# Optimization experiments

Hardware: AMD Instinct MI355X
Metric: run time of the kernel (lower is better)

## Reference

```python
import jax, jax.numpy as jnp
import numpy as np

B, S, D, H = 2, 4096, 512, 8
HD = D // H  # 64


def setup_inputs() -> dict:
    key = jax.random.key(0)
    ks = jax.random.split(key, 9)
    def lin_init(kw, kb, fan_in, fan_out):
        bound = 1.0 / np.sqrt(fan_in)
        W = jax.random.uniform(kw, (fan_in, fan_out), minval=-bound, maxval=bound, dtype=jnp.float32)
        b = jax.random.uniform(kb, (fan_out,), minval=-bound, maxval=bound, dtype=jnp.float32)
        return W, b
    Wq, bq = lin_init(ks[0], ks[1], D, D)
    Wk, bk = lin_init(ks[2], ks[3], D, D)
    Wv, bv = lin_init(ks[4], ks[5], D, D)
    query = jax.random.normal(ks[6], (B, S, D), dtype=jnp.float32)
    key_in = jax.random.normal(ks[7], (B, S, D), dtype=jnp.float32)
    value = jax.random.normal(ks[8], (B, S, D), dtype=jnp.float32)
    return {"query": query, "key": key_in, "value": value,
            "Wq": Wq, "bq": bq, "Wk": Wk, "bk": bk, "Wv": Wv, "bv": bv}


def _split_heads(x):
    # [B, S, D] -> [B, H, S, HD]
    b, s, _ = x.shape
    return x.reshape(b, s, H, HD).transpose(0, 2, 1, 3)


def reference(query, key, value, Wq, bq, Wk, bk, Wv, bv):
    Q = _split_heads(query @ Wq + bq)
    K = _split_heads(key @ Wk + bk)
    V = _split_heads(value @ Wv + bv)
    scale = 1.0 / np.sqrt(HD).astype(np.float32)
    # scores: [B, H, Sq, Sk]
    scores = jnp.einsum('bhqd,bhkd->bhqk', Q, K) * scale
    weights = jax.nn.softmax(scores, axis=-1)
    att = jnp.einsum('bhqk,bhkd->bhqd', weights, V)
    # [B, H, S, HD] -> [B, S, D]
    return att.transpose(0, 2, 1, 3).reshape(query.shape[0], query.shape[1], D)
```

## Files before the change

kernel.cpp:

```cpp
#include <hip/hip_runtime.h>
#include <hip/hip_bf16.h>
#include <cstdint>


typedef __bf16   bf16x8 __attribute__((ext_vector_type(8)));
typedef _Float16 f16x8  __attribute__((ext_vector_type(8)));
typedef float    f32x4  __attribute__((ext_vector_type(4)));
typedef float    f32x16 __attribute__((ext_vector_type(16)));
typedef unsigned int   u32;
typedef unsigned int   u32x4 __attribute__((ext_vector_type(4)));
typedef unsigned short u16;

#define NB  2
#define SEQ 4096
#define DIM 512
#define NH  8
#define HD  64
#define WSZ (DIM * DIM)
#define XSZ (NB * SEQ * DIM)
#define QSZ (NB * NH * SEQ * HD)

__device__ __forceinline__ u16 f2bf(float f) {
    __bf16 h = (__bf16)f; return __builtin_bit_cast(u16, h);
}
__device__ __forceinline__ u16 f2h(float f) {
    _Float16 h = (_Float16)f; return __builtin_bit_cast(u16, h);
}
__device__ __forceinline__ u32 pack_pkrtz(float a, float b) {
    auto pk = __builtin_amdgcn_cvt_pkrtz(a, b);
    return __builtin_bit_cast(u32, pk);
}
__device__ __forceinline__ bf16x8 cvt8p(float4 a, float4 b) {
    bf16x8 o;
    o[0]=(__bf16)a.x; o[1]=(__bf16)a.y; o[2]=(__bf16)a.z; o[3]=(__bf16)a.w;
    o[4]=(__bf16)b.x; o[5]=(__bf16)b.y; o[6]=(__bf16)b.z; o[7]=(__bf16)b.w;
    return o;
}
__device__ __forceinline__ void dma16(const u16* g, u16* l) {
    __builtin_amdgcn_global_load_lds(
        (const __attribute__((address_space(1))) u32*)g,
        (__attribute__((address_space(3))) u32*)l, 16, 0, 0);
}

__global__ __launch_bounds__(256) void xcvt_kernel(
    const float* __restrict__ xq, const float* __restrict__ xk,
    const float* __restrict__ xv, u16* __restrict__ xb)
{
    const int id = blockIdx.x;
    const int p = id >> 10, rest = id & 1023;
    const int mtile = rest >> 4, kk = rest & 15;
    const float* X = (p == 0) ? xq : ((p == 1) ? xk : xv);
    const int t = threadIdx.x;
    const int row = t >> 1, half = t & 1;
    const float* src = X + ((size_t)(mtile * 128 + row)) * DIM + kk * 32 + half * 16;
    u16* dst = xb + (size_t)p * XSZ + ((size_t)(mtile * 16 + kk)) * 4096 + row * 32;
    const int sr = (row ^ (row >> 2)) & 3;
    float4 a0 = ((const float4*)src)[0], a1 = ((const float4*)src)[1];
    float4 a2 = ((const float4*)src)[2], a3 = ((const float4*)src)[3];
    const int c0 = (half * 2) ^ sr, c1 = (half * 2 + 1) ^ sr;
    *(bf16x8*)(dst + (c0 << 3)) = cvt8p(a0, a1);
    *(bf16x8*)(dst + (c1 << 3)) = cvt8p(a2, a3);
}

__global__ __launch_bounds__(256) void wt_kernel(
    const float* __restrict__ Wq, const float* __restrict__ Wk,
    const float* __restrict__ Wv, u16* __restrict__ wtImg)
{
    __shared__ u16 lT[64 * 65];
    const int p = blockIdx.z;
    const float* W = (p == 0) ? Wq : ((p == 1) ? Wk : Wv);
    const int r0 = blockIdx.x * 64, c0 = blockIdx.y * 64;
    const int t = threadIdx.x;
#pragma unroll
    for (int i = 0; i < 16; i++) {
        int idx = i * 256 + t, rowk = idx >> 6, coln = idx & 63;
        lT[coln * 65 + rowk] = f2bf(W[(size_t)(r0 + rowk) * DIM + c0 + coln]);
    }
    __syncthreads();
#pragma unroll
    for (int i = 0; i < 2; i++) {
        const int idx = i * 256 + t;
        const int nl = idx >> 3, ch = idx & 7;
        const int n = c0 + nl;
        const int row = n & 127, ntile = n >> 7;
        const int kk = (r0 >> 5) + (ch >> 2);
        const int sw = (ch & 3) ^ ((row ^ (row >> 2)) & 3);
        u16* d = wtImg + (size_t)p * WSZ + ((size_t)(ntile * 16 + kk)) * 4096
               + row * 32 + (sw << 3);
#pragma unroll
        for (int e = 0; e < 8; e++) d[e] = lT[nl * 65 + ch * 8 + e];
    }
}

__global__ __launch_bounds__(256) void proj_kernel(
    const u16* __restrict__ xb, const u16* __restrict__ wtImg,
    const float* __restrict__ bq, const float* __restrict__ bk,
    const float* __restrict__ bv,
    u16* __restrict__ qb, u16* __restrict__ kbImg, u16* __restrict__ vtImg)
{
    __shared__ u16 smem[16384];

    const int tid = threadIdx.x;
    const int wave = tid >> 6, lane = tid & 63;
    const int l16 = lane & 15, quad = lane >> 4;
    const int wq = wave >> 1, wn = wave & 1;

    const int id = blockIdx.x;
    const int xcd = id & 7, j = id >> 3;
    const int p = j >> 5, t5 = j & 31;
    int mb, nb;
    if (p < 2) { mb = xcd * 8 + (t5 >> 2); nb = t5 & 3; }
    else       { nb = xcd * 8 + (t5 >> 2); mb = t5 & 3; }

    const u16* Abase = (p < 2) ? xb + (size_t)p * XSZ + (size_t)mb * 16 * 4096
                               : wtImg + (size_t)2 * WSZ + (size_t)mb * 16 * 4096;
    const u16* Bbase = (p < 2) ? wtImg + (size_t)p * WSZ + (size_t)nb * 16 * 4096
                               : xb + (size_t)2 * XSZ + (size_t)nb * 16 * 4096;
    const int doff = tid * 8;

    f32x4 acc[4][4];
#pragma unroll
    for (int ms = 0; ms < 4; ms++)
#pragma unroll
        for (int ns = 0; ns < 4; ns++)
#pragma unroll
            for (int jj = 0; jj < 4; jj++) acc[ms][ns][jj] = 0.f;

#pragma unroll
    for (int e = 0; e < 2; e++) {
        dma16(Abase + e * 2048 + doff, smem + e * 2048 + doff);
        dma16(Bbase + e * 2048 + doff, smem + 4096 + e * 2048 + doff);
    }
    Abase += 4096; Bbase += 4096;

    for (int kt = 0; kt < 16; kt++) {
        __syncthreads();
        if (kt < 15) {
            u16* lb = smem + ((kt + 1) & 1) * 8192;
#pragma unroll
            for (int e = 0; e < 2; e++) {
                dma16(Abase + e * 2048 + doff, lb + e * 2048 + doff);
                dma16(Bbase + e * 2048 + doff, lb + 4096 + e * 2048 + doff);
            }
            Abase += 4096; Bbase += 4096;
        }
        const u16* lA = smem + (kt & 1) * 8192;
        const u16* lB = lA + 4096;

        bf16x8 af[4];
#pragma unroll
        for (int ms = 0; ms < 4; ms++) {
            const int row = wq * 64 + ms * 16 + l16;
            const int sr = (row ^ (row >> 2)) & 3;
            af[ms] = *(const bf16x8*)&lA[row * 32 + ((quad ^ sr) << 3)];
        }
#pragma unroll
        for (int ns = 0; ns < 4; ns++) {
            const int rowb = wn * 64 + ns * 16 + l16;
            const int sb = (rowb ^ (rowb >> 2)) & 3;
            const bf16x8 b = *(const bf16x8*)&lB[rowb * 32 + ((quad ^ sb) << 3)];
#pragma unroll
            for (int ms = 0; ms < 4; ms++)
                acc[ms][ns] = __builtin_amdgcn_mfma_f32_16x16x32_bf16(af[ms], b, acc[ms][ns], 0, 0, 0);
        }
    }

    __syncthreads();
    if (p < 2) {
        const float* bias = p ? bk : bq;
        const float cs = (p == 0) ? 0.18033688011112042f : 1.0f;
        const int stl = wn * 2 + wq;
        const int hh = nb * 2 + wn;
#pragma unroll
        for (int ns = 0; ns < 4; ns++) {
            const int ch = ns * 16 + l16;
            const float bval = bias[hh * 64 + ch];
#pragma unroll
            for (int ms = 0; ms < 4; ms++)
#pragma unroll
                for (int rr = 0; rr < 4; rr++) {
                    const int sqL = ms * 16 + quad * 4 + rr;
                    const float v = (acc[ms][ns][rr] + bval) * cs;
                    int off;
                    if (p == 0) off = sqL * 64 + ch;
                    else        off = sqL * 64 +
                                      (((ch >> 3) ^ ((sqL ^ (sqL >> 3)) & 7)) << 3) + (ch & 7);
                    smem[stl * 4096 + off] = f2bf(v);
                }
        }
    } else {
        const int stl = wq * 2 + wn;
#pragma unroll
        for (int ms = 0; ms < 4; ms++)
#pragma unroll
            for (int rr = 0; rr < 4; rr++) {
                const int hd = ms * 16 + quad * 4 + rr;
                const float bval = bv[mb * 128 + wq * 64 + hd];
                const int swh = (hd ^ (hd >> 3)) & 7;
#pragma unroll
                for (int ns = 0; ns < 4; ns++) {
                    const int nl = ns * 16 + l16;
                    const int sqpL = (nl & ~12) | ((nl & 8) >> 1) | ((nl & 4) << 1);
                    smem[stl * 4096 + hd * 64 +
                         (((sqpL >> 3) ^ swh) << 3) + (sqpL & 7)] =
                        f2h(acc[ms][ns][rr] + bval);
                }
            }
    }
    __syncthreads();

    {
        u16* dstp; size_t gbase;
        if (p < 2) {
            const int hh = nb * 2 + (wave >> 1);
            const int b2 = mb >> 5;
            const int row0 = (mb * 128 + (wave & 1) * 64) & 4095;
            if (p == 0) { dstp = qb;    gbase = ((size_t)(b2 * NH + hh) * 4096 + row0) * 64; }
            else        { dstp = kbImg; gbase = ((size_t)((b2 * NH + hh) * 64 + (row0 >> 6))) * 4096; }
        } else {
            const int hh = mb * 2 + (wave >> 1);
            const int b2 = nb >> 5;
            const int nblk = (nb & 31) * 2 + (wave & 1);
            dstp = vtImg; gbase = ((size_t)((b2 * NH + hh) * 64 + nblk)) * 4096;
        }
#pragma unroll
        for (int e = 0; e < 8; e++) {
            const u32x4 vv = *(const u32x4*)&smem[wave * 4096 + e * 512 + lane * 8];
            *(u32x4*)(dstp + gbase + e * 512 + lane * 8) = vv;
        }
    }
}

__global__ __launch_bounds__(512, 4) void attn_kernel(
    const u16* __restrict__ qb, const u16* __restrict__ kbImg,
    const u16* __restrict__ vtImg, float* __restrict__ out)
{
    __shared__ u16 smem[2 * 4 * 4096];
    float* cmb = (float*)smem;

    const int tid = threadIdx.x;
    const int wave = tid >> 6, lane = tid & 63;
    const int m31 = lane & 31, h = lane >> 5;
    const int wq = wave >> 1, kh = wave & 1;

    const int blk = blockIdx.x;
    const int xcd = blk & 7, idx = blk >> 3;
    const int bh = xcd * 2 + (idx >> 5);
    const int qt = idx & 31;
    const int qbase = qt * 128 + wq * 32;

    bf16x8 qF[4];
#pragma unroll
    for (int c = 0; c < 4; c++)
        qF[c] = *(const bf16x8*)(qb + ((size_t)bh * SEQ + qbase + m31) * HD + c * 16 + h * 8);

    f32x16 O0, O1;
#pragma unroll
    for (int j = 0; j < 16; j++) { O0[j] = 0.f; O1[j] = 0.f; }
    float l_acc = 0.f;

    const int st  = wave >> 1;
    const int hw  = wave & 1;
    const u16* img = (st & 1) ? vtImg : kbImg;
    const u16* gp = img + ((size_t)(bh * 64 + (st >> 1) * 32)) * 4096 + hw * 2048 + lane * 8;
    {
        u16* lb = smem + st * 4096 + hw * 2048 + lane * 8;
#pragma unroll
        for (int e = 0; e < 4; e++) dma16(gp + e * 512, lb + e * 512);
        gp += 4096;
    }

    const int NT = 32;
    for (int it = 0; it < NT; it++) {
        __syncthreads();
        if (it + 1 < NT) {
            u16* lb = smem + ((((it + 1) & 1) * 4 + st)) * 4096 + hw * 2048 + lane * 8;
#pragma unroll
            for (int e = 0; e < 4; e++) dma16(gp + e * 512, lb + e * 512);
            gp += 4096;
        }
        const u16* sK = smem + (size_t)(((it & 1) * 4) + kh * 2) * 4096;
        const u16* sV = sK + 4096;

#pragma unroll
        for (int kg = 0; kg < 2; kg++) {
            const int rK = kg * 32 + m31;
            const int swK = (rK ^ (rK >> 3)) & 7;
            bf16x8 kA[4];
#pragma unroll
            for (int c = 0; c < 4; c++)
                kA[c] = *(const bf16x8*)&sK[(rK << 6) + (((2 * c + h) ^ swK) << 3)];

            const int swV0 = (m31 ^ (m31 >> 3)) & 7;
            const int rV1 = 32 + m31;
            const int swV1 = (rV1 ^ (rV1 >> 3)) & 7;
            f16x8 vA0[2], vA1[2];
#pragma unroll
            for (int c2 = 0; c2 < 2; c2++) {
                vA0[c2] = *(const f16x8*)&sV[(m31 << 6) + (((4 * kg + 2 * c2 + h) ^ swV0) << 3)];
                vA1[c2] = *(const f16x8*)&sV[(rV1 << 6) + (((4 * kg + 2 * c2 + h) ^ swV1) << 3)];
            }

            f32x16 Sv;
#pragma unroll
            for (int j = 0; j < 16; j++) Sv[j] = 0.f;
#pragma unroll
            for (int c = 0; c < 4; c++)
                Sv = __builtin_amdgcn_mfma_f32_32x32x16_bf16(kA[c], qF[c], Sv, 0, 0, 0);

            float ps = 0.f;
            u32 P32[8];
#pragma unroll
            for (int mm = 0; mm < 8; mm++) {
                const float e0 = __builtin_amdgcn_exp2f(Sv[2 * mm]);
                const float e1 = __builtin_amdgcn_exp2f(Sv[2 * mm + 1]);
                ps += e0 + e1;
                P32[mm] = pack_pkrtz(e0, e1);
            }
            l_acc += ps;

            u32x4 f0, f1;
            f0[0] = P32[0]; f0[1] = P32[1]; f0[2] = P32[2]; f0[3] = P32[3];
            f1[0] = P32[4]; f1[1] = P32[5]; f1[2] = P32[6]; f1[3] = P32[7];
            const f16x8 pf0 = __builtin_bit_cast(f16x8, f0);
            const f16x8 pf1 = __builtin_bit_cast(f16x8, f1);
            O0 = __builtin_amdgcn_mfma_f32_32x32x16_f16(vA0[0], pf0, O0, 0, 0, 0);
            O0 = __builtin_amdgcn_mfma_f32_32x32x16_f16(vA0[1], pf1, O0, 0, 0, 0);
            O1 = __builtin_amdgcn_mfma_f32_32x32x16_f16(vA1[0], pf0, O1, 0, 0, 0);
            O1 = __builtin_amdgcn_mfma_f32_32x32x16_f16(vA1[1], pf1, O1, 0, 0, 0);
        }
    }

    l_acc += __shfl_xor(l_acc, 32);
    __syncthreads();
    if (kh == 1) {
#pragma unroll
        for (int hg = 0; hg < 2; hg++)
#pragma unroll
            for (int mm = 0; mm < 4; mm++) {
                f32x4 o;
#pragma unroll
                for (int j = 0; j < 4; j++) o[j] = (hg ? O1 : O0)[4 * mm + j];
                *(f32x4*)&cmb[(((wq * 2 + hg) * 4 + mm) << 8) + lane * 4] = o;
            }
        cmb[8192 + wq * 64 + lane] = l_acc;
    }
    __syncthreads();

    if (kh == 0) {
        const int b = bh >> 3, hcol = bh & 7;
        const float lt = l_acc + cmb[8192 + wq * 64 + lane];
        const float inv = 1.0f / lt;
        const int sq = qbase + m31;
#pragma unroll
        for (int hg = 0; hg < 2; hg++)
#pragma unroll
            for (int mm = 0; mm < 4; mm++) {
                const f32x4 po = *(const f32x4*)&cmb[(((wq * 2 + hg) * 4 + mm) << 8) + lane * 4];
                f32x4 o;
#pragma unroll
                for (int j = 0; j < 4; j++)
                    o[j] = ((hg ? O1 : O0)[4 * mm + j] + po[j]) * inv;
                *(f32x4*)&out[(((size_t)(b * SEQ + sq)) << 9) + hcol * 64
                              + hg * 32 + 8 * mm + 4 * h] = o;
            }
    }
}

extern "C" void kernel_launch(void* const* d_in, const int* in_sizes, int n_in,
                              void* d_out, int out_size, void* d_ws, size_t ws_size,
                              hipStream_t stream)
{
    const float* q  = (const float*)d_in[0];
    const float* k  = (const float*)d_in[1];
    const float* v  = (const float*)d_in[2];
    const float* Wq = (const float*)d_in[3];
    const float* bq = (const float*)d_in[4];
    const float* Wk = (const float*)d_in[5];
    const float* bk = (const float*)d_in[6];
    const float* Wv = (const float*)d_in[7];
    const float* bv = (const float*)d_in[8];
    float* out = (float*)d_out;

    u16* xb  = (u16*)d_ws;
    u16* wti = xb  + (size_t)3 * XSZ;
    u16* qbp = wti + (size_t)3 * WSZ;
    u16* kbp = qbp + (size_t)QSZ;
    u16* vtp = kbp + (size_t)QSZ;

    xcvt_kernel<<<dim3(3072),   256, 0, stream>>>(q, k, v, xb);
    wt_kernel  <<<dim3(8, 8, 3), 256, 0, stream>>>(Wq, Wk, Wv, wti);
    proj_kernel<<<dim3(768),    256, 0, stream>>>(xb, wti, bq, bk, bv,
                                                  qbp, kbp, vtp);
    attn_kernel<<<dim3(512),    512, 0, stream>>>(qbp, kbp, vtp, out);
}
```

Before: 211.2 us.

## Split attention KV work across 4 waves per query tile and merge prep kernels

Attention blocks grow from 512 to 1024 threads, so each query group is served by four key-split waves instead of two. Each wave handles one 32-key sub-tile per iteration rather than looping over two, which gives more waves to hide latency. The partial outputs and row sums are combined with a two-stage reduction through shared memory. The input-conversion and weight-transpose kernels are merged into one launch, MFMA sections get s_setprio hints, and the row sum is accumulated with fdot2 on the packed f16 probabilities. In exchange, the reduction epilogue is larger and the launch bounds put more register pressure on each thread.

```diff
diff --git a/kernel.cpp b/kernel.cpp
--- a/kernel.cpp
+++ b/kernel.cpp
@@ -5,6 +5,7 @@
 
 typedef __bf16   bf16x8 __attribute__((ext_vector_type(8)));
 typedef _Float16 f16x8  __attribute__((ext_vector_type(8)));
+typedef _Float16 f16x2  __attribute__((ext_vector_type(2)));
 typedef float    f32x4  __attribute__((ext_vector_type(4)));
 typedef float    f32x16 __attribute__((ext_vector_type(16)));
 typedef unsigned int   u32;
@@ -20,6 +21,12 @@
 #define XSZ (NB * SEQ * DIM)
 #define QSZ (NB * NH * SEQ * HD)
 
+#if __has_builtin(__builtin_amdgcn_fdot2)
+#define HAVE_FDOT2 1
+#else
+#define HAVE_FDOT2 0
+#endif
+
 __device__ __forceinline__ u16 f2bf(float f) {
     __bf16 h = (__bf16)f; return __builtin_bit_cast(u16, h);
 }
@@ -42,53 +49,53 @@
         (__attribute__((address_space(3))) u32*)l, 16, 0, 0);
 }
 
-__global__ __launch_bounds__(256) void xcvt_kernel(
+__global__ __launch_bounds__(256) void prep_kernel(
     const float* __restrict__ xq, const float* __restrict__ xk,
-    const float* __restrict__ xv, u16* __restrict__ xb)
-{
-    const int id = blockIdx.x;
-    const int p = id >> 10, rest = id & 1023;
-    const int mtile = rest >> 4, kk = rest & 15;
-    const float* X = (p == 0) ? xq : ((p == 1) ? xk : xv);
-    const int t = threadIdx.x;
-    const int row = t >> 1, half = t & 1;
-    const float* src = X + ((size_t)(mtile * 128 + row)) * DIM + kk * 32 + half * 16;
-    u16* dst = xb + (size_t)p * XSZ + ((size_t)(mtile * 16 + kk)) * 4096 + row * 32;
-    const int sr = (row ^ (row >> 2)) & 3;
-    float4 a0 = ((const float4*)src)[0], a1 = ((const float4*)src)[1];
-    float4 a2 = ((const float4*)src)[2], a3 = ((const float4*)src)[3];
-    const int c0 = (half * 2) ^ sr, c1 = (half * 2 + 1) ^ sr;
-    *(bf16x8*)(dst + (c0 << 3)) = cvt8p(a0, a1);
-    *(bf16x8*)(dst + (c1 << 3)) = cvt8p(a2, a3);
-}
-
-__global__ __launch_bounds__(256) void wt_kernel(
+    const float* __restrict__ xv,
     const float* __restrict__ Wq, const float* __restrict__ Wk,
-    const float* __restrict__ Wv, u16* __restrict__ wtImg)
+    const float* __restrict__ Wv,
+    u16* __restrict__ xb, u16* __restrict__ wtImg)
 {
     __shared__ u16 lT[64 * 65];
-    const int p = blockIdx.z;
-    const float* W = (p == 0) ? Wq : ((p == 1) ? Wk : Wv);
-    const int r0 = blockIdx.x * 64, c0 = blockIdx.y * 64;
+    const int id = blockIdx.x;
     const int t = threadIdx.x;
-#pragma unroll
-    for (int i = 0; i < 16; i++) {
-        int idx = i * 256 + t, rowk = idx >> 6, coln = idx & 63;
-        lT[coln * 65 + rowk] = f2bf(W[(size_t)(r0 + rowk) * DIM + c0 + coln]);
-    }
-    __syncthreads();
-#pragma unroll
-    for (int i = 0; i < 2; i++) {
-        const int idx = i * 256 + t;
-        const int nl = idx >> 3, ch = idx & 7;
-        const int n = c0 + nl;
-        const int row = n & 127, ntile = n >> 7;
-        const int kk = (r0 >> 5) + (ch >> 2);
-        const int sw = (ch & 3) ^ ((row ^ (row >> 2)) & 3);
-        u16* d = wtImg + (size_t)p * WSZ + ((size_t)(ntile * 16 + kk)) * 4096
-               + row * 32 + (sw << 3);
-#pragma unroll
-        for (int e = 0; e < 8; e++) d[e] = lT[nl * 65 + ch * 8 + e];
+    if (id < 3072) {
+        const int p = id >> 10, rest = id & 1023;
+        const int mtile = rest >> 4, kk = rest & 15;
+        const float* X = (p == 0) ? xq : ((p == 1) ? xk : xv);
+        const int row = t >> 1, half = t & 1;
+        const float* src = X + ((size_t)(mtile * 128 + row)) * DIM + kk * 32 + half * 16;
+        u16* dst = xb + (size_t)p * XSZ + ((size_t)(mtile * 16 + kk)) * 4096 + row * 32;
+        const int sr = (row ^ (row >> 2)) & 3;
+        float4 a0 = ((const float4*)src)[0], a1 = ((const float4*)src)[1];
+        float4 a2 = ((const float4*)src)[2], a3 = ((const float4*)src)[3];
+        const int c0 = (half * 2) ^ sr, c1 = (half * 2 + 1) ^ sr;
+        *(bf16x8*)(dst + (c0 << 3)) = cvt8p(a0, a1);
+        *(bf16x8*)(dst + (c1 << 3)) = cvt8p(a2, a3);
+    } else {
+        const int id2 = id - 3072;
+        const int p = id2 >> 6;
+        const float* W = (p == 0) ? Wq : ((p == 1) ? Wk : Wv);
+        const int r0 = ((id2 >> 3) & 7) * 64, c0 = (id2 & 7) * 64;
+#pragma unroll
+        for (int i = 0; i < 16; i++) {
+            int idx = i * 256 + t, rowk = idx >> 6, coln = idx & 63;
+            lT[coln * 65 + rowk] = f2bf(W[(size_t)(r0 + rowk) * DIM + c0 + coln]);
+        }
+        __syncthreads();
+#pragma unroll
+        for (int i = 0; i < 2; i++) {
+            const int idx = i * 256 + t;
+            const int nl = idx >> 3, ch = idx & 7;
+            const int n = c0 + nl;
+            const int row = n & 127, ntile = n >> 7;
+            const int kk = (r0 >> 5) + (ch >> 2);
+            const int sw = (ch & 3) ^ ((row ^ (row >> 2)) & 3);
+            u16* d = wtImg + (size_t)p * WSZ + ((size_t)(ntile * 16 + kk)) * 4096
+                   + row * 32 + (sw << 3);
+#pragma unroll
+            for (int e = 0; e < 8; e++) d[e] = lT[nl * 65 + ch * 8 + e];
+        }
     }
 }
 
@@ -231,17 +238,17 @@
     }
 }
 
-__global__ __launch_bounds__(512, 4) void attn_kernel(
+__global__ __launch_bounds__(1024, 8) void attn_kernel(
     const u16* __restrict__ qb, const u16* __restrict__ kbImg,
     const u16* __restrict__ vtImg, float* __restrict__ out)
 {
-    __shared__ u16 smem[2 * 4 * 4096];
-    float* cmb = (float*)smem;
+    __shared__ u16 smem[2 * 16384];
+    float* sf = (float*)smem;
 
     const int tid = threadIdx.x;
     const int wave = tid >> 6, lane = tid & 63;
     const int m31 = lane & 31, h = lane >> 5;
-    const int wq = wave >> 1, kh = wave & 1;
+    const int wq = wave >> 2, kh = wave & 3;
 
     const int blk = blockIdx.x;
     const int xcd = blk & 7, idx = blk >> 3;
@@ -257,106 +264,139 @@
     f32x16 O0, O1;
 #pragma unroll
     for (int j = 0; j < 16; j++) { O0[j] = 0.f; O1[j] = 0.f; }
-    float l_acc = 0.f;
-
-    const int st  = wave >> 1;
-    const int hw  = wave & 1;
-    const u16* img = (st & 1) ? vtImg : kbImg;
-    const u16* gp = img + ((size_t)(bh * 64 + (st >> 1) * 32)) * 4096 + hw * 2048 + lane * 8;
-    {
-        u16* lb = smem + st * 4096 + hw * 2048 + lane * 8;
-#pragma unroll
-        for (int e = 0; e < 4; e++) dma16(gp + e * 512, lb + e * 512);
-        gp += 4096;
-    }
+    float la_ = 0.f, lb_ = 0.f;
+#if HAVE_FDOT2
+    const f16x2 one2 = {(_Float16)1.f, (_Float16)1.f};
+#endif
+
+    const int region = wave >> 3, sub8 = wave & 7;
+    const u16* img = region ? vtImg : kbImg;
+    const u16* gp = img + ((size_t)(bh * 64)) * 4096 + sub8 * 1024 + lane * 8;
+    u16* const lds0 = smem + region * 8192 + sub8 * 1024 + lane * 8;
+
+    dma16(gp, lds0); dma16(gp + 512, lds0 + 512);
+    gp += 8192;
 
     const int NT = 32;
     for (int it = 0; it < NT; it++) {
         __syncthreads();
         if (it + 1 < NT) {
-            u16* lb = smem + ((((it + 1) & 1) * 4 + st)) * 4096 + hw * 2048 + lane * 8;
-#pragma unroll
-            for (int e = 0; e < 4; e++) dma16(gp + e * 512, lb + e * 512);
-            gp += 4096;
-        }
-        const u16* sK = smem + (size_t)(((it & 1) * 4) + kh * 2) * 4096;
-        const u16* sV = sK + 4096;
-
-#pragma unroll
-        for (int kg = 0; kg < 2; kg++) {
-            const int rK = kg * 32 + m31;
-            const int swK = (rK ^ (rK >> 3)) & 7;
-            bf16x8 kA[4];
-#pragma unroll
-            for (int c = 0; c < 4; c++)
-                kA[c] = *(const bf16x8*)&sK[(rK << 6) + (((2 * c + h) ^ swK) << 3)];
-
-            const int swV0 = (m31 ^ (m31 >> 3)) & 7;
-            const int rV1 = 32 + m31;
-            const int swV1 = (rV1 ^ (rV1 >> 3)) & 7;
-            f16x8 vA0[2], vA1[2];
-#pragma unroll
-            for (int c2 = 0; c2 < 2; c2++) {
-                vA0[c2] = *(const f16x8*)&sV[(m31 << 6) + (((4 * kg + 2 * c2 + h) ^ swV0) << 3)];
-                vA1[c2] = *(const f16x8*)&sV[(rV1 << 6) + (((4 * kg + 2 * c2 + h) ^ swV1) << 3)];
+            u16* ld = lds0 + ((it + 1) & 1) * 16384;
+            dma16(gp, ld); dma16(gp + 512, ld + 512);
+            gp += 8192;
+        }
+        const u16* sb = smem + (it & 1) * 16384;
+        const u16* sK = sb + ((kh >> 1) << 12);
+        const u16* sV = sb + 8192 + ((kh >> 1) << 12);
+
+        const int rK = ((kh & 1) << 5) + m31;
+        const int swK = (rK ^ (rK >> 3)) & 7;
+        bf16x8 kA[4];
+#pragma unroll
+        for (int c = 0; c < 4; c++)
+            kA[c] = *(const bf16x8*)&sK[(rK << 6) + (((2 * c + h) ^ swK) << 3)];
+
+        f32x16 Sv;
+#pragma unroll
+        for (int j = 0; j < 16; j++) Sv[j] = 0.f;
+        __builtin_amdgcn_s_setprio(1);
+#pragma unroll
+        for (int c = 0; c < 4; c++)
+            Sv = __builtin_amdgcn_mfma_f32_32x32x16_bf16(kA[c], qF[c], Sv, 0, 0, 0);
+        __builtin_amdgcn_s_setprio(0);
+
+        const int gb = (kh & 1) << 2;
+        const int swV0 = (m31 ^ (m31 >> 3)) & 7;
+        const int rV1 = 32 + m31;
+        const int swV1 = (rV1 ^ (rV1 >> 3)) & 7;
+        f16x8 vA0[2], vA1[2];
+#pragma unroll
+        for (int c2 = 0; c2 < 2; c2++) {
+            vA0[c2] = *(const f16x8*)&sV[(m31 << 6) + (((gb + 2 * c2 + h) ^ swV0) << 3)];
+            vA1[c2] = *(const f16x8*)&sV[(rV1 << 6) + (((gb + 2 * c2 + h) ^ swV1) << 3)];
+        }
+
+        u32 P32[8];
+#pragma unroll
+        for (int mm = 0; mm < 8; mm++) {
+            const float ea = __builtin_amdgcn_exp2f(Sv[2 * mm]);
+            const float eb = __builtin_amdgcn_exp2f(Sv[2 * mm + 1]);
+            P32[mm] = pack_pkrtz(ea, eb);
+#if HAVE_FDOT2
+            const f16x2 pp = __builtin_bit_cast(f16x2, P32[mm]);
+            if (mm & 1) lb_ = __builtin_amdgcn_fdot2(pp, one2, lb_, false);
+            else        la_ = __builtin_amdgcn_fdot2(pp, one2, la_, false);
+#else
+            if (mm & 1) lb_ += ea + eb; else la_ += ea + eb;
+#endif
+        }
+
+        u32x4 f0, f1;
+        f0[0] = P32[0]; f0[1] = P32[1]; f0[2] = P32[2]; f0[3] = P32[3];
+        f1[0] = P32[4]; f1[1] = P32[5]; f1[2] = P32[6]; f1[3] = P32[7];
+        const f16x8 pf0 = __builtin_bit_cast(f16x8, f0);
+        const f16x8 pf1 = __builtin_bit_cast(f16x8, f1);
+        __builtin_amdgcn_s_setprio(1);
+        O0 = __builtin_amdgcn_mfma_f32_32x32x16_f16(vA0[0], pf0, O0, 0, 0, 0);
+        O0 = __builtin_amdgcn_mfma_f32_32x32x16_f16(vA0[1], pf1, O0, 0, 0, 0);
+        O1 = __builtin_amdgcn_mfma_f32_32x32x16_f16(vA1[0], pf0, O1, 0, 0, 0);
+        O1 = __builtin_amdgcn_mfma_f32_32x32x16_f16(vA1[1], pf1, O1, 0, 0, 0);
+        __builtin_amdgcn_s_setprio(0);
+    }
+
+    float l_acc = la_ + lb_;
+    l_acc += __shfl_xor(l_acc, 32);
+
+    if (lane < 32) sf[wave * 32 + lane] = l_acc;
+    __syncthreads();
+    const float lt = sf[(wq * 4 + 0) * 32 + m31] + sf[(wq * 4 + 1) * 32 + m31]
+                   + sf[(wq * 4 + 2) * 32 + m31] + sf[(wq * 4 + 3) * 32 + m31];
+    const float inv = 1.0f / lt;
+    __syncthreads();
+
+    if (kh >= 2) {
+        const int w2 = wq * 2 + (kh - 2);
+#pragma unroll
+        for (int s = 0; s < 8; s++) {
+            f32x4 tv;
+#pragma unroll
+            for (int j = 0; j < 4; j++) tv[j] = (s < 4 ? O0 : O1)[(s & 3) * 4 + j];
+            *(f32x4*)&sf[w2 * 2048 + s * 256 + lane * 4] = tv;
+        }
+    }
+    __syncthreads();
+    if (kh < 2) {
+        const int w2 = wq * 2 + kh;
+#pragma unroll
+        for (int s = 0; s < 8; s++) {
+            const f32x4 tv = *(const f32x4*)&sf[w2 * 2048 + s * 256 + lane * 4];
+#pragma unroll
+            for (int j = 0; j < 4; j++) {
+                if (s < 4) O0[(s & 3) * 4 + j] += tv[j];
+                else       O1[(s & 3) * 4 + j] += tv[j];
             }
-
-            f32x16 Sv;
-#pragma unroll
-            for (int j = 0; j < 16; j++) Sv[j] = 0.f;
-#pragma unroll
-            for (int c = 0; c < 4; c++)
-                Sv = __builtin_amdgcn_mfma_f32_32x32x16_bf16(kA[c], qF[c], Sv, 0, 0, 0);
-
-            float ps = 0.f;
-            u32 P32[8];
-#pragma unroll
-            for (int mm = 0; mm < 8; mm++) {
-                const float e0 = __builtin_amdgcn_exp2f(Sv[2 * mm]);
-                const float e1 = __builtin_amdgcn_exp2f(Sv[2 * mm + 1]);
-                ps += e0 + e1;
-                P32[mm] = pack_pkrtz(e0, e1);
-            }
-            l_acc += ps;
-
-            u32x4 f0, f1;
-            f0[0] = P32[0]; f0[1] = P32[1]; f0[2] = P32[2]; f0[3] = P32[3];
-            f1[0] = P32[4]; f1[1] = P32[5]; f1[2] = P32[6]; f1[3] = P32[7];
-            const f16x8 pf0 = __builtin_bit_cast(f16x8, f0);
-            const f16x8 pf1 = __builtin_bit_cast(f16x8, f1);
-            O0 = __builtin_amdgcn_mfma_f32_32x32x16_f16(vA0[0], pf0, O0, 0, 0, 0);
-            O0 = __builtin_amdgcn_mfma_f32_32x32x16_f16(vA0[1], pf1, O0, 0, 0, 0);
-            O1 = __builtin_amdgcn_mfma_f32_32x32x16_f16(vA1[0], pf0, O1, 0, 0, 0);
-            O1 = __builtin_amdgcn_mfma_f32_32x32x16_f16(vA1[1], pf1, O1, 0, 0, 0);
-        }
-    }
-
-    l_acc += __shfl_xor(l_acc, 32);
+        }
+    }
     __syncthreads();
     if (kh == 1) {
 #pragma unroll
-        for (int hg = 0; hg < 2; hg++)
-#pragma unroll
-            for (int mm = 0; mm < 4; mm++) {
-                f32x4 o;
-#pragma unroll
-                for (int j = 0; j < 4; j++) o[j] = (hg ? O1 : O0)[4 * mm + j];
-                *(f32x4*)&cmb[(((wq * 2 + hg) * 4 + mm) << 8) + lane * 4] = o;
-            }
-        cmb[8192 + wq * 64 + lane] = l_acc;
-    }
-    __syncthreads();
-
+        for (int s = 0; s < 8; s++) {
+            f32x4 tv;
+#pragma unroll
+            for (int j = 0; j < 4; j++) tv[j] = (s < 4 ? O0 : O1)[(s & 3) * 4 + j];
+            *(f32x4*)&sf[wq * 2048 + s * 256 + lane * 4] = tv;
+        }
+    }
+    __syncthreads();
     if (kh == 0) {
         const int b = bh >> 3, hcol = bh & 7;
-        const float lt = l_acc + cmb[8192 + wq * 64 + lane];
-        const float inv = 1.0f / lt;
         const int sq = qbase + m31;
 #pragma unroll
         for (int hg = 0; hg < 2; hg++)
 #pragma unroll
             for (int mm = 0; mm < 4; mm++) {
-                const f32x4 po = *(const f32x4*)&cmb[(((wq * 2 + hg) * 4 + mm) << 8) + lane * 4];
+                const int s = hg * 4 + mm;
+                const f32x4 po = *(const f32x4*)&sf[wq * 2048 + s * 256 + lane * 4];
                 f32x4 o;
 #pragma unroll
                 for (int j = 0; j < 4; j++)
@@ -388,9 +428,8 @@
     u16* kbp = qbp + (size_t)QSZ;
     u16* vtp = kbp + (size_t)QSZ;
 
-    xcvt_kernel<<<dim3(3072),   256, 0, stream>>>(q, k, v, xb);
-    wt_kernel  <<<dim3(8, 8, 3), 256, 0, stream>>>(Wq, Wk, Wv, wti);
-    proj_kernel<<<dim3(768),    256, 0, stream>>>(xb, wti, bq, bk, bv,
-                                                  qbp, kbp, vtp);
-    attn_kernel<<<dim3(512),    512, 0, stream>>>(qbp, kbp, vtp, out);
-}
+    prep_kernel<<<dim3(3264), 256, 0, stream>>>(q, k, v, Wq, Wk, Wv, xb, wti);
+    proj_kernel<<<dim3(768),  256, 0, stream>>>(xb, wti, bq, bk, bv,
+                                                qbp, kbp, vtp);
+    attn_kernel<<<dim3(512), 1024, 0, stream>>>(qbp, kbp, vtp, out);
+}
```

Measured after the change: 771.7 us. 3.65x slower.

## Merge prep kernels and software-pipeline QK/PV MFMAs in attention loop

Applied to the files above, without the earlier changes.

Merges the input-conversion and weight-transpose kernels into one launch, removing a kernel launch and its tail. In the attention inner loop, the two key groups are manually unrolled so the second group's QK MFMAs are interleaved with the first group's PV MFMAs. MFMA sections are wrapped in s_setprio, and the row-sum is accumulated with fdot2 on packed fp16 into two accumulators. The aim is to overlap exp/VALU work with matrix ops and cut launch overhead. The costs are higher register pressure and slightly different rounding in the row-sum.

```diff
diff --git a/kernel.cpp b/kernel.cpp
--- a/kernel.cpp
+++ b/kernel.cpp
@@ -5,6 +5,7 @@
 
 typedef __bf16   bf16x8 __attribute__((ext_vector_type(8)));
 typedef _Float16 f16x8  __attribute__((ext_vector_type(8)));
+typedef _Float16 f16x2  __attribute__((ext_vector_type(2)));
 typedef float    f32x4  __attribute__((ext_vector_type(4)));
 typedef float    f32x16 __attribute__((ext_vector_type(16)));
 typedef unsigned int   u32;
@@ -20,6 +21,12 @@
 #define XSZ (NB * SEQ * DIM)
 #define QSZ (NB * NH * SEQ * HD)
 
+#if __has_builtin(__builtin_amdgcn_fdot2)
+#define HAVE_FDOT2 1
+#else
+#define HAVE_FDOT2 0
+#endif
+
 __device__ __forceinline__ u16 f2bf(float f) {
     __bf16 h = (__bf16)f; return __builtin_bit_cast(u16, h);
 }
@@ -42,53 +49,53 @@
         (__attribute__((address_space(3))) u32*)l, 16, 0, 0);
 }
 
-__global__ __launch_bounds__(256) void xcvt_kernel(
+__global__ __launch_bounds__(256) void prep_kernel(
     const float* __restrict__ xq, const float* __restrict__ xk,
-    const float* __restrict__ xv, u16* __restrict__ xb)
-{
-    const int id = blockIdx.x;
-    const int p = id >> 10, rest = id & 1023;
-    const int mtile = rest >> 4, kk = rest & 15;
-    const float* X = (p == 0) ? xq : ((p == 1) ? xk : xv);
-    const int t = threadIdx.x;
-    const int row = t >> 1, half = t & 1;
-    const float* src = X + ((size_t)(mtile * 128 + row)) * DIM + kk * 32 + half * 16;
-    u16* dst = xb + (size_t)p * XSZ + ((size_t)(mtile * 16 + kk)) * 4096 + row * 32;
-    const int sr = (row ^ (row >> 2)) & 3;
-    float4 a0 = ((const float4*)src)[0], a1 = ((const float4*)src)[1];
-    float4 a2 = ((const float4*)src)[2], a3 = ((const float4*)src)[3];
-    const int c0 = (half * 2) ^ sr, c1 = (half * 2 + 1) ^ sr;
-    *(bf16x8*)(dst + (c0 << 3)) = cvt8p(a0, a1);
-    *(bf16x8*)(dst + (c1 << 3)) = cvt8p(a2, a3);
-}
-
-__global__ __launch_bounds__(256) void wt_kernel(
+    const float* __restrict__ xv,
     const float* __restrict__ Wq, const float* __restrict__ Wk,
-    const float* __restrict__ Wv, u16* __restrict__ wtImg)
+    const float* __restrict__ Wv,
+    u16* __restrict__ xb, u16* __restrict__ wtImg)
 {
     __shared__ u16 lT[64 * 65];
-    const int p = blockIdx.z;
-    const float* W = (p == 0) ? Wq : ((p == 1) ? Wk : Wv);
-    const int r0 = blockIdx.x * 64, c0 = blockIdx.y * 64;
+    const int id = blockIdx.x;
     const int t = threadIdx.x;
-#pragma unroll
-    for (int i = 0; i < 16; i++) {
-        int idx = i * 256 + t, rowk = idx >> 6, coln = idx & 63;
-        lT[coln * 65 + rowk] = f2bf(W[(size_t)(r0 + rowk) * DIM + c0 + coln]);
-    }
-    __syncthreads();
-#pragma unroll
-    for (int i = 0; i < 2; i++) {
-        const int idx = i * 256 + t;
-        const int nl = idx >> 3, ch = idx & 7;
-        const int n = c0 + nl;
-        const int row = n & 127, ntile = n >> 7;
-        const int kk = (r0 >> 5) + (ch >> 2);
-        const int sw = (ch & 3) ^ ((row ^ (row >> 2)) & 3);
-        u16* d = wtImg + (size_t)p * WSZ + ((size_t)(ntile * 16 + kk)) * 4096
-               + row * 32 + (sw << 3);
-#pragma unroll
-        for (int e = 0; e < 8; e++) d[e] = lT[nl * 65 + ch * 8 + e];
+    if (id < 3072) {
+        const int p = id >> 10, rest = id & 1023;
+        const int mtile = rest >> 4, kk = rest & 15;
+        const float* X = (p == 0) ? xq : ((p == 1) ? xk : xv);
+        const int row = t >> 1, half = t & 1;
+        const float* src = X + ((size_t)(mtile * 128 + row)) * DIM + kk * 32 + half * 16;
+        u16* dst = xb + (size_t)p * XSZ + ((size_t)(mtile * 16 + kk)) * 4096 + row * 32;
+        const int sr = (row ^ (row >> 2)) & 3;
+        float4 a0 = ((const float4*)src)[0], a1 = ((const float4*)src)[1];
+        float4 a2 = ((const float4*)src)[2], a3 = ((const float4*)src)[3];
+        const int c0 = (half * 2) ^ sr, c1 = (half * 2 + 1) ^ sr;
+        *(bf16x8*)(dst + (c0 << 3)) = cvt8p(a0, a1);
+        *(bf16x8*)(dst + (c1 << 3)) = cvt8p(a2, a3);
+    } else {
+        const int id2 = id - 3072;
+        const int p = id2 >> 6;
+        const float* W = (p == 0) ? Wq : ((p == 1) ? Wk : Wv);
+        const int r0 = ((id2 >> 3) & 7) * 64, c0 = (id2 & 7) * 64;
+#pragma unroll
+        for (int i = 0; i < 16; i++) {
+            int idx = i * 256 + t, rowk = idx >> 6, coln = idx & 63;
+            lT[coln * 65 + rowk] = f2bf(W[(size_t)(r0 + rowk) * DIM + c0 + coln]);
+        }
+        __syncthreads();
+#pragma unroll
+        for (int i = 0; i < 2; i++) {
+            const int idx = i * 256 + t;
+            const int nl = idx >> 3, ch = idx & 7;
+            const int n = c0 + nl;
+            const int row = n & 127, ntile = n >> 7;
+            const int kk = (r0 >> 5) + (ch >> 2);
+            const int sw = (ch & 3) ^ ((row ^ (row >> 2)) & 3);
+            u16* d = wtImg + (size_t)p * WSZ + ((size_t)(ntile * 16 + kk)) * 4096
+                   + row * 32 + (sw << 3);
+#pragma unroll
+            for (int e = 0; e < 8; e++) d[e] = lT[nl * 65 + ch * 8 + e];
+        }
     }
 }
 
@@ -257,7 +264,10 @@
     f32x16 O0, O1;
 #pragma unroll
     for (int j = 0; j < 16; j++) { O0[j] = 0.f; O1[j] = 0.f; }
-    float l_acc = 0.f;
+    float la_ = 0.f, lb_ = 0.f;
+#if HAVE_FDOT2
+    const f16x2 one2 = {(_Float16)1.f, (_Float16)1.f};
+#endif
 
     const int st  = wave >> 1;
     const int hw  = wave & 1;
@@ -270,6 +280,14 @@
         gp += 4096;
     }
 
+    const int swV0 = (m31 ^ (m31 >> 3)) & 7;
+    const int rV1  = 32 + m31;
+    const int swV1 = (rV1 ^ (rV1 >> 3)) & 7;
+    const int rK0  = m31;
+    const int swK0 = (rK0 ^ (rK0 >> 3)) & 7;
+    const int rK1  = 32 + m31;
+    const int swK1 = (rK1 ^ (rK1 >> 3)) & 7;
+
     const int NT = 32;
     for (int it = 0; it < NT; it++) {
         __syncthreads();
@@ -282,55 +300,103 @@
         const u16* sK = smem + (size_t)(((it & 1) * 4) + kh * 2) * 4096;
         const u16* sV = sK + 4096;
 
-#pragma unroll
-        for (int kg = 0; kg < 2; kg++) {
-            const int rK = kg * 32 + m31;
-            const int swK = (rK ^ (rK >> 3)) & 7;
-            bf16x8 kA[4];
-#pragma unroll
-            for (int c = 0; c < 4; c++)
-                kA[c] = *(const bf16x8*)&sK[(rK << 6) + (((2 * c + h) ^ swK) << 3)];
-
-            const int swV0 = (m31 ^ (m31 >> 3)) & 7;
-            const int rV1 = 32 + m31;
-            const int swV1 = (rV1 ^ (rV1 >> 3)) & 7;
-            f16x8 vA0[2], vA1[2];
-#pragma unroll
-            for (int c2 = 0; c2 < 2; c2++) {
-                vA0[c2] = *(const f16x8*)&sV[(m31 << 6) + (((4 * kg + 2 * c2 + h) ^ swV0) << 3)];
-                vA1[c2] = *(const f16x8*)&sV[(rV1 << 6) + (((4 * kg + 2 * c2 + h) ^ swV1) << 3)];
-            }
-
-            f32x16 Sv;
-#pragma unroll
-            for (int j = 0; j < 16; j++) Sv[j] = 0.f;
-#pragma unroll
-            for (int c = 0; c < 4; c++)
-                Sv = __builtin_amdgcn_mfma_f32_32x32x16_bf16(kA[c], qF[c], Sv, 0, 0, 0);
-
-            float ps = 0.f;
-            u32 P32[8];
-#pragma unroll
-            for (int mm = 0; mm < 8; mm++) {
-                const float e0 = __builtin_amdgcn_exp2f(Sv[2 * mm]);
-                const float e1 = __builtin_amdgcn_exp2f(Sv[2 * mm + 1]);
-                ps += e0 + e1;
-                P32[mm] = pack_pkrtz(e0, e1);
-            }
-            l_acc += ps;
-
-            u32x4 f0, f1;
-            f0[0] = P32[0]; f0[1] = P32[1]; f0[2] = P32[2]; f0[3] = P32[3];
-            f1[0] = P32[4]; f1[1] = P32[5]; f1[2] = P32[6]; f1[3] = P32[7];
-            const f16x8 pf0 = __builtin_bit_cast(f16x8, f0);
-            const f16x8 pf1 = __builtin_bit_cast(f16x8, f1);
-            O0 = __builtin_amdgcn_mfma_f32_32x32x16_f16(vA0[0], pf0, O0, 0, 0, 0);
-            O0 = __builtin_amdgcn_mfma_f32_32x32x16_f16(vA0[1], pf1, O0, 0, 0, 0);
-            O1 = __builtin_amdgcn_mfma_f32_32x32x16_f16(vA1[0], pf0, O1, 0, 0, 0);
-            O1 = __builtin_amdgcn_mfma_f32_32x32x16_f16(vA1[1], pf1, O1, 0, 0, 0);
-        }
-    }
-
+        bf16x8 kA0[4];
+#pragma unroll
+        for (int c = 0; c < 4; c++)
+            kA0[c] = *(const bf16x8*)&sK[(rK0 << 6) + (((2 * c + h) ^ swK0) << 3)];
+
+        f32x16 Sv0;
+#pragma unroll
+        for (int j = 0; j < 16; j++) Sv0[j] = 0.f;
+        __builtin_amdgcn_s_setprio(1);
+#pragma unroll
+        for (int c = 0; c < 4; c++)
+            Sv0 = __builtin_amdgcn_mfma_f32_32x32x16_bf16(kA0[c], qF[c], Sv0, 0, 0, 0);
+        __builtin_amdgcn_s_setprio(0);
+
+        f16x8 vA00[2], vA01[2];
+#pragma unroll
+        for (int c2 = 0; c2 < 2; c2++) {
+            vA00[c2] = *(const f16x8*)&sV[(m31 << 6) + (((2 * c2 + h) ^ swV0) << 3)];
+            vA01[c2] = *(const f16x8*)&sV[(rV1 << 6) + (((2 * c2 + h) ^ swV1) << 3)];
+        }
+
+        u32 P0[8];
+#pragma unroll
+        for (int mm = 0; mm < 8; mm++) {
+            const float ea = __builtin_amdgcn_exp2f(Sv0[2 * mm]);
+            const float eb = __builtin_amdgcn_exp2f(Sv0[2 * mm + 1]);
+            P0[mm] = pack_pkrtz(ea, eb);
+#if HAVE_FDOT2
+            const f16x2 pp = __builtin_bit_cast(f16x2, P0[mm]);
+            if (mm & 1) lb_ = __builtin_amdgcn_fdot2(pp, one2, lb_, false);
+            else        la_ = __builtin_amdgcn_fdot2(pp, one2, la_, false);
+#else
+            if (mm & 1) lb_ += ea + eb; else la_ += ea + eb;
+#endif
+        }
+        u32x4 g0, g1;
+        g0[0] = P0[0]; g0[1] = P0[1]; g0[2] = P0[2]; g0[3] = P0[3];
+        g1[0] = P0[4]; g1[1] = P0[5]; g1[2] = P0[6]; g1[3] = P0[7];
+        const f16x8 pf00 = __builtin_bit_cast(f16x8, g0);
+        const f16x8 pf01 = __builtin_bit_cast(f16x8, g1);
+
+        bf16x8 kA1[4];
+#pragma unroll
+        for (int c = 0; c < 4; c++)
+            kA1[c] = *(const bf16x8*)&sK[(rK1 << 6) + (((2 * c + h) ^ swK1) << 3)];
+
+        f32x16 Sv1;
+#pragma unroll
+        for (int j = 0; j < 16; j++) Sv1[j] = 0.f;
+
+        __builtin_amdgcn_s_setprio(1);
+        Sv1 = __builtin_amdgcn_mfma_f32_32x32x16_bf16(kA1[0], qF[0], Sv1, 0, 0, 0);
+        O0  = __builtin_amdgcn_mfma_f32_32x32x16_f16(vA00[0], pf00, O0, 0, 0, 0);
+        Sv1 = __builtin_amdgcn_mfma_f32_32x32x16_bf16(kA1[1], qF[1], Sv1, 0, 0, 0);
+        O0  = __builtin_amdgcn_mfma_f32_32x32x16_f16(vA00[1], pf01, O0, 0, 0, 0);
+        Sv1 = __builtin_amdgcn_mfma_f32_32x32x16_bf16(kA1[2], qF[2], Sv1, 0, 0, 0);
+        O1  = __builtin_amdgcn_mfma_f32_32x32x16_f16(vA01[0], pf00, O1, 0, 0, 0);
+        Sv1 = __builtin_amdgcn_mfma_f32_32x32x16_bf16(kA1[3], qF[3], Sv1, 0, 0, 0);
+        O1  = __builtin_amdgcn_mfma_f32_32x32x16_f16(vA01[1], pf01, O1, 0, 0, 0);
+        __builtin_amdgcn_s_setprio(0);
+
+        f16x8 vA10[2], vA11[2];
+#pragma unroll
+        for (int c2 = 0; c2 < 2; c2++) {
+            vA10[c2] = *(const f16x8*)&sV[(m31 << 6) + (((4 + 2 * c2 + h) ^ swV0) << 3)];
+            vA11[c2] = *(const f16x8*)&sV[(rV1 << 6) + (((4 + 2 * c2 + h) ^ swV1) << 3)];
+        }
+
+        u32 P1[8];
+#pragma unroll
+        for (int mm = 0; mm < 8; mm++) {
+            const float ea = __builtin_amdgcn_exp2f(Sv1[2 * mm]);
+            const float eb = __builtin_amdgcn_exp2f(Sv1[2 * mm + 1]);
+            P1[mm] = pack_pkrtz(ea, eb);
+#if HAVE_FDOT2
+            const f16x2 pp = __builtin_bit_cast(f16x2, P1[mm]);
+            if (mm & 1) lb_ = __builtin_amdgcn_fdot2(pp, one2, lb_, false);
+            else        la_ = __builtin_amdgcn_fdot2(pp, one2, la_, false);
+#else
+            if (mm & 1) lb_ += ea + eb; else la_ += ea + eb;
+#endif
+        }
+        u32x4 h0, h1;
+        h0[0] = P1[0]; h0[1] = P1[1]; h0[2] = P1[2]; h0[3] = P1[3];
+        h1[0] = P1[4]; h1[1] = P1[5]; h1[2] = P1[6]; h1[3] = P1[7];
+        const f16x8 pf10 = __builtin_bit_cast(f16x8, h0);
+        const f16x8 pf11 = __builtin_bit_cast(f16x8, h1);
+
+        __builtin_amdgcn_s_setprio(1);
+        O0 = __builtin_amdgcn_mfma_f32_32x32x16_f16(vA10[0], pf10, O0, 0, 0, 0);
+        O0 = __builtin_amdgcn_mfma_f32_32x32x16_f16(vA10[1], pf11, O0, 0, 0, 0);
+        O1 = __builtin_amdgcn_mfma_f32_32x32x16_f16(vA11[0], pf10, O1, 0, 0, 0);
+        O1 = __builtin_amdgcn_mfma_f32_32x32x16_f16(vA11[1], pf11, O1, 0, 0, 0);
+        __builtin_amdgcn_s_setprio(0);
+    }
+
+    float l_acc = la_ + lb_;
     l_acc += __shfl_xor(l_acc, 32);
     __syncthreads();
     if (kh == 1) {
@@ -388,9 +454,8 @@
     u16* kbp = qbp + (size_t)QSZ;
     u16* vtp = kbp + (size_t)QSZ;
 
-    xcvt_kernel<<<dim3(3072),   256, 0, stream>>>(q, k, v, xb);
-    wt_kernel  <<<dim3(8, 8, 3), 256, 0, stream>>>(Wq, Wk, Wv, wti);
-    proj_kernel<<<dim3(768),    256, 0, stream>>>(xb, wti, bq, bk, bv,
-                                                  qbp, kbp, vtp);
-    attn_kernel<<<dim3(512),    512, 0, stream>>>(qbp, kbp, vtp, out);
-}
+    prep_kernel<<<dim3(3264), 256, 0, stream>>>(q, k, v, Wq, Wk, Wv, xb, wti);
+    proj_kernel<<<dim3(768),  256, 0, stream>>>(xb, wti, bq, bk, bv,
+                                                qbp, kbp, vtp);
+    attn_kernel<<<dim3(512),  512, 0, stream>>>(qbp, kbp, vtp, out);
+}
```

Measured after the change: 202.5 us. 1.04x faster.
